# Optimization experiments

Measured on AMD Instinct MI355X. Metric: run time of the kernel, lower is better.

The kernel has to match this reference:

```python
import jax, jax.numpy as jnp
import numpy as np

N = 50000
E = 800000
D_IN, D_HID, D_OUT = 128, 128, 64


def setup_inputs() -> dict:
    key = jax.random.key(0)
    ks = jax.random.split(key, 8)
    x = jax.random.normal(ks[0], (N, D_IN), dtype=jnp.float32)
    edge_index = jax.random.randint(ks[1], (2, E), 0, N, dtype=jnp.int64)
    # Glorot-ish init for weights
    W1 = jax.random.normal(ks[2], (D_IN, D_HID), dtype=jnp.float32) / np.sqrt(D_IN)
    b1 = jnp.zeros((D_HID,), dtype=jnp.float32)
    W2 = jax.random.normal(ks[3], (D_HID, D_OUT), dtype=jnp.float32) / np.sqrt(D_HID)
    b2 = jnp.zeros((D_OUT,), dtype=jnp.float32)
    fc_W = jax.random.normal(ks[4], (D_OUT, D_OUT), dtype=jnp.float32) / np.sqrt(D_OUT)
    fc_b = jnp.zeros((D_OUT,), dtype=jnp.float32)
    return {"x": x, "edge_index": edge_index, "W1": W1, "b1": b1,
            "W2": W2, "b2": b2, "fc_W": fc_W, "fc_b": fc_b}


def _gcn_norm(edge_index, n_nodes):
    # PyG GCNConv default: add self-loops, symmetric normalization
    src, dst = edge_index[0], edge_index[1]
    loops = jnp.arange(n_nodes, dtype=edge_index.dtype)
    src = jnp.concatenate([src, loops])
    dst = jnp.concatenate([dst, loops])
    deg = jax.ops.segment_sum(jnp.ones_like(dst, dtype=jnp.float32), dst,
                              num_segments=n_nodes)
    dinv = jnp.where(deg > 0, jax.lax.rsqrt(deg), 0.0)
    norm = dinv[src] * dinv[dst]  # [E + N]
    return src, dst, norm


def _gcn_conv(x, src, dst, norm, W, b):
    h = x @ W                          # [N, d_out] transform first (fewer FLOPs)
    msg = h[src] * norm[:, None]       # gather + scale  [E+N, d_out]
    out = jax.ops.segment_sum(msg, dst, num_segments=x.shape[0])
    return out + b


def reference(x, edge_index, W1, b1, W2, b2, fc_W, fc_b):
    src, dst, norm = _gcn_norm(edge_index, x.shape[0])
    h = jax.nn.relu(_gcn_conv(x, src, dst, norm, W1, b1))
    h = jax.nn.relu(_gcn_conv(h, src, dst, norm, W2, b2))
    return h @ fc_W + fc_b
```

## Files before the change

kernel.cpp:

```cpp
#include <hip/hip_runtime.h>
#include <hip/hip_bf16.h>


typedef __attribute__((ext_vector_type(8))) short bf16x8;
typedef __attribute__((ext_vector_type(4))) float f32x4;

#define SLAB 64
#define BCAP 6144
#define BINCH 8192

__device__ __forceinline__ unsigned short f2bf(float f) {
    unsigned u = __float_as_uint(f);
    unsigned r = (u + 0x7FFFu + ((u >> 16) & 1u)) >> 16;
    return (unsigned short)r;
}
__device__ __forceinline__ float bf16_lo(unsigned u) {
    return __uint_as_float((u & 0xFFFFu) << 16);
}
__device__ __forceinline__ float bf16_hi(unsigned u) {
    return __uint_as_float(u & 0xFFFF0000u);
}

#define UNPK16(cA, cB, ci)                                        \
    ci[0] = cA.x & 0xFFFFu;  ci[1] = cA.x >> 16;                  \
    ci[2] = cA.y & 0xFFFFu;  ci[3] = cA.y >> 16;                  \
    ci[4] = cA.z & 0xFFFFu;  ci[5] = cA.z >> 16;                  \
    ci[6] = cA.w & 0xFFFFu;  ci[7] = cA.w >> 16;                  \
    ci[8] = cB.x & 0xFFFFu;  ci[9] = cB.x >> 16;                  \
    ci[10] = cB.y & 0xFFFFu; ci[11] = cB.y >> 16;                 \
    ci[12] = cB.z & 0xFFFFu; ci[13] = cB.z >> 16;                 \
    ci[14] = cB.w & 0xFFFFu; ci[15] = cB.w >> 16;


__global__ void k_wt(const float* __restrict__ W1, const float* __restrict__ W2,
                     const float* __restrict__ fcW,
                     unsigned short* __restrict__ W1T, unsigned short* __restrict__ W2T,
                     unsigned short* __restrict__ fcWT, int* __restrict__ gcnt,
                     unsigned short* __restrict__ hs1r, unsigned short* __restrict__ hs2,
                     int n) {
    int j = blockIdx.x * blockDim.x + threadIdx.x;
    if (j < 256) gcnt[j] = 0;
    if (j < 16384) {
        int m = j >> 7, k = j & 127;
        W1T[j] = f2bf(W1[k * 128 + m]);
    } else if (j < 24576) {
        int q = j - 16384;
        int m = q >> 7, k = q & 127;
        W2T[q] = f2bf(W2[k * 64 + m]);
    } else if (j < 28672) {
        int q = j - 24576;
        int m = q >> 6, k = q & 63;
        fcWT[q] = f2bf(fcW[k * 64 + m]);
    } else if (j < 28800) {
        hs1r[(size_t)n * 128 + (j - 28672)] = 0;
    } else if (j < 28864) {
        hs2[(size_t)n * 64 + (j - 28800)] = 0;
    }
}


__device__ __forceinline__ void gemm1_body(const float* __restrict__ X,
                                           const unsigned short* __restrict__ W1T,
                                           unsigned short* __restrict__ outp,
                                           int n, int blk, int tid,
                                           unsigned short* xs) {
    constexpr int LDW = 136;
    int base = blk * 64;
    for (int idx = tid; idx < 64 * 32; idx += 256) {
        int r = idx >> 5, c = idx & 31;
        int row = base + r;
        float4 v = make_float4(0.f, 0.f, 0.f, 0.f);
        if (row < n) v = ((const float4*)X)[(size_t)row * 32 + c];
        unsigned short* dp = &xs[r * LDW + c * 4];
        dp[0] = f2bf(v.x); dp[1] = f2bf(v.y); dp[2] = f2bf(v.z); dp[3] = f2bf(v.w);
    }
    __syncthreads();

    int wave = tid >> 6, lane = tid & 63;
    int quad = lane >> 4, l16 = lane & 15;
    int rbase = wave * 16;

    bf16x8 af[4];
#pragma unroll
    for (int kb = 0; kb < 4; ++kb)
        af[kb] = *(const bf16x8*)&xs[(rbase + l16) * LDW + kb * 32 + quad * 8];

#pragma unroll
    for (int jt = 0; jt < 8; ++jt) {
        f32x4 acc = {0.f, 0.f, 0.f, 0.f};
#pragma unroll
        for (int kb = 0; kb < 4; ++kb) {
            bf16x8 bf = *(const bf16x8*)&W1T[(size_t)(jt * 16 + l16) * 128 + kb * 32 + quad * 8];
            acc = __builtin_amdgcn_mfma_f32_16x16x32_bf16(af[kb], bf, acc, 0, 0, 0);
        }
#pragma unroll
        for (int r = 0; r < 4; ++r) {
            int row = base + rbase + quad * 4 + r;
            if (row < n)
                outp[(size_t)row * 128 + jt * 16 + l16] = f2bf(acc[r]);
        }
    }
}


__global__ __launch_bounds__(1024) void k_front(
    const int* __restrict__ src, const int* __restrict__ dst, int e,
    int* __restrict__ gcnt, unsigned* __restrict__ staging,
    const float* __restrict__ x, const unsigned short* __restrict__ W1T,
    unsigned short* __restrict__ hs1r, int n, int nbk, int ngemm) {
    __shared__ __align__(16) unsigned short xs4[4][64 * 136];
    __shared__ int bcnt[256], bpos[256], gofs[256];
    int bid = (int)blockIdx.x, tid = (int)threadIdx.x;

    if (bid < ngemm) {
        int tile = tid >> 8;
        gemm1_body(x, W1T, hs1r, n, bid * 4 + tile, tid & 255, xs4[tile]);
    } else {
        int b0 = bid - ngemm;
        if (tid < 256) { bcnt[tid] = 0; bpos[tid] = 0; }
        __syncthreads();
        int e0 = b0 * BINCH;
        int d[8], s[8];
#pragma unroll
        for (int r = 0; r < 8; ++r) {
            int i = e0 + r * 1024 + tid;
            if (i < e) { d[r] = dst[i]; s[r] = src[i]; } else d[r] = -1;
        }
#pragma unroll
        for (int r = 0; r < 8; ++r)
            if (d[r] >= 0) atomicAdd(&bcnt[d[r] >> 8], 1);
        __syncthreads();
        if (tid < nbk) {
            int c = bcnt[tid];
            gofs[tid] = c ? atomicAdd(&gcnt[tid], c) : 0;
        }
        __syncthreads();
#pragma unroll
        for (int r = 0; r < 8; ++r) {
            if (d[r] >= 0) {
                int b = d[r] >> 8;
                int p = atomicAdd(&bpos[b], 1);
                int idx = gofs[b] + p;
                if (idx < BCAP)
                    staging[(size_t)b * BCAP + idx] =
                        ((unsigned)d[r] << 16) | (unsigned)s[r];
            }
        }
    }
}


__global__ __launch_bounds__(1024) void k_scatter(
    const unsigned* __restrict__ staging, const int* __restrict__ gcnt,
    int* __restrict__ cnt, unsigned short* __restrict__ col,
    float* __restrict__ dinv, unsigned* __restrict__ hs1u, int n) {
    __shared__ int lcnt[256];
    __shared__ __align__(16) unsigned short ls[256 * SLAB];
    __shared__ float sdi[256];
    int b = (int)blockIdx.x, t = (int)threadIdx.x;
    if (t < 256) lcnt[t] = 0;
    unsigned sent2 = (unsigned)n | ((unsigned)n << 16);
    for (int i = t; i < 256 * SLAB / 2; i += 1024) ((unsigned*)ls)[i] = sent2;
    __syncthreads();
    int eb = gcnt[b]; if (eb > BCAP) eb = BCAP;
    const unsigned* sp = staging + (size_t)b * BCAP;
    for (int i = t; i < eb; i += 1024) {
        unsigned pk = sp[i];
        int dl = (int)(pk >> 16) & 255;
        int pos = atomicAdd(&lcnt[dl], 1);
        if (pos < SLAB) ls[(dl << 6) + pos] = (unsigned short)(pk & 0xFFFFu);
    }
    __syncthreads();
    int base = b << 8;
    const uint4* lsv = (const uint4*)ls;
    uint4* gv = (uint4*)(col + ((size_t)base << 6));
    for (int i = t; i < 256 * SLAB / 8; i += 1024) gv[i] = lsv[i];
    if (t < 256) {
        int c = lcnt[t];
        float dv = rsqrtf((float)c + 1.0f);
        sdi[t] = dv;
        cnt[base + t] = c;
        dinv[base + t] = dv;
    }
    __syncthreads();
    int rows = n - base; if (rows > 256) rows = 256; if (rows < 0) rows = 0;
    unsigned* hp = hs1u + ((size_t)base << 6);
    for (int i = t; i < rows * 64; i += 1024) {
        int r = i >> 6;
        unsigned u = hp[i];
        float sc = sdi[r];
        unsigned lo = f2bf(sc * bf16_lo(u));
        unsigned hi = f2bf(sc * bf16_hi(u));
        hp[i] = lo | (hi << 16);
    }
}


__global__ __launch_bounds__(256) void k_aggg128(
    const int* __restrict__ cnt, const unsigned short* __restrict__ col,
    const unsigned short* __restrict__ hs, const float* __restrict__ dinv,
    const float* __restrict__ bias, const unsigned short* __restrict__ W2T,
    unsigned short* __restrict__ hs2, int n) {
    __shared__ __align__(16) unsigned short ys[16 * 136];
    __shared__ float ldi[16];
    int tid = (int)threadIdx.x;
    int w = tid >> 6, lane = tid & 63;
    int q = lane >> 4, l16 = lane & 15;
    int gbase = (int)blockIdx.x * 16;
    const uint4* hp4 = (const uint4*)hs;

    int node = gbase + w * 4 + q;
    int c = cnt[node]; if (c > SLAB) c = SLAB;
    int dm = c;
    int o = __shfl_xor(dm, 16); if (o > dm) dm = o;
    o = __shfl_xor(dm, 32); if (o > dm) dm = o;

    const unsigned short* cp = &col[(size_t)node * SLAB];
    float di = dinv[node];
    int h0 = node < n ? node : n;
    uint4 su = hp4[(size_t)h0 * 16 + l16];
    float a0 = bf16_lo(su.x), a1 = bf16_hi(su.x);
    float a2 = bf16_lo(su.y), a3 = bf16_hi(su.y);
    float a4 = bf16_lo(su.z), a5 = bf16_hi(su.z);
    float a6 = bf16_lo(su.w), a7 = bf16_hi(su.w);

    for (int i = 0; i < dm; i += 16) {
        uint4 cA = *(const uint4*)&cp[i];
        uint4 cB = *(const uint4*)&cp[i + 8];
        unsigned ci[16];
        UNPK16(cA, cB, ci)
        uint4 u[16];
#pragma unroll
        for (int j = 0; j < 16; ++j) u[j] = hp4[(size_t)ci[j] * 16 + l16];
#pragma unroll
        for (int j = 0; j < 16; ++j) {
            a0 += bf16_lo(u[j].x); a1 += bf16_hi(u[j].x);
            a2 += bf16_lo(u[j].y); a3 += bf16_hi(u[j].y);
            a4 += bf16_lo(u[j].z); a5 += bf16_hi(u[j].z);
            a6 += bf16_lo(u[j].w); a7 += bf16_hi(u[j].w);
        }
    }

    float4 bv0 = *(const float4*)&bias[l16 * 8];
    float4 bv1 = *(const float4*)&bias[l16 * 8 + 4];
    float v0 = fmaxf(di * a0 + bv0.x, 0.0f);
    float v1 = fmaxf(di * a1 + bv0.y, 0.0f);
    float v2 = fmaxf(di * a2 + bv0.z, 0.0f);
    float v3 = fmaxf(di * a3 + bv0.w, 0.0f);
    float v4 = fmaxf(di * a4 + bv1.x, 0.0f);
    float v5 = fmaxf(di * a5 + bv1.y, 0.0f);
    float v6 = fmaxf(di * a6 + bv1.z, 0.0f);
    float v7 = fmaxf(di * a7 + bv1.w, 0.0f);
    uint4 ov;
    ov.x = (unsigned)f2bf(v0) | ((unsigned)f2bf(v1) << 16);
    ov.y = (unsigned)f2bf(v2) | ((unsigned)f2bf(v3) << 16);
    ov.z = (unsigned)f2bf(v4) | ((unsigned)f2bf(v5) << 16);
    ov.w = (unsigned)f2bf(v6) | ((unsigned)f2bf(v7) << 16);
    *(uint4*)((char*)ys + (size_t)(w * 4 + q) * 272 + l16 * 16) = ov;
    if (l16 == 0) ldi[w * 4 + q] = di;
    __syncthreads();

    int quad = lane >> 4, l16b = lane & 15;
    bf16x8 a[4];
#pragma unroll
    for (int kb = 0; kb < 4; ++kb)
        a[kb] = *(const bf16x8*)&ys[l16b * 136 + kb * 32 + quad * 8];
    f32x4 acc = {0.f, 0.f, 0.f, 0.f};
#pragma unroll
    for (int kb = 0; kb < 4; ++kb) {
        bf16x8 bf = *(const bf16x8*)&W2T[(size_t)(w * 16 + l16b) * 128 + kb * 32 + quad * 8];
        acc = __builtin_amdgcn_mfma_f32_16x16x32_bf16(a[kb], bf, acc, 0, 0, 0);
    }
#pragma unroll
    for (int r = 0; r < 4; ++r) {
        int lrow = quad * 4 + r;
        int row = gbase + lrow;
        if (row < n)
            hs2[(size_t)row * 64 + w * 16 + l16b] = f2bf(acc[r] * ldi[lrow]);
    }
}


__global__ __launch_bounds__(256) void k_aggg64(
    const int* __restrict__ cnt, const unsigned short* __restrict__ col,
    const unsigned short* __restrict__ hs, const float* __restrict__ dinv,
    const float* __restrict__ bias, const unsigned short* __restrict__ fcWT,
    const float* __restrict__ fcb, float* __restrict__ out, int n) {
    __shared__ __align__(16) unsigned short yt[16 * 72];
    int tid = (int)threadIdx.x;
    int w = tid >> 6, lane = tid & 63;
    int q = lane >> 4, l16 = lane & 15;
    int gbase = (int)blockIdx.x * 16;
    const uint2* hp2 = (const uint2*)hs;

    int node = gbase + w * 4 + q;
    int c = cnt[node]; if (c > SLAB) c = SLAB;
    int dm = c;
    int o = __shfl_xor(dm, 16); if (o > dm) dm = o;
    o = __shfl_xor(dm, 32); if (o > dm) dm = o;

    const unsigned short* cp = &col[(size_t)node * SLAB];
    float di = dinv[node];
    int h0 = node < n ? node : n;
    uint2 su = hp2[(size_t)h0 * 16 + l16];
    float a0 = bf16_lo(su.x), a1 = bf16_hi(su.x);
    float a2 = bf16_lo(su.y), a3 = bf16_hi(su.y);

    for (int i = 0; i < dm; i += 16) {
        uint4 cA = *(const uint4*)&cp[i];
        uint4 cB = *(const uint4*)&cp[i + 8];
        unsigned ci[16];
        UNPK16(cA, cB, ci)
        uint2 u[16];
#pragma unroll
        for (int j = 0; j < 16; ++j) u[j] = hp2[(size_t)ci[j] * 16 + l16];
#pragma unroll
        for (int j = 0; j < 16; ++j) {
            a0 += bf16_lo(u[j].x); a1 += bf16_hi(u[j].x);
            a2 += bf16_lo(u[j].y); a3 += bf16_hi(u[j].y);
        }
    }

    float4 bv = *(const float4*)&bias[l16 * 4];
    float v0 = fmaxf(di * a0 + bv.x, 0.0f);
    float v1 = fmaxf(di * a1 + bv.y, 0.0f);
    float v2 = fmaxf(di * a2 + bv.z, 0.0f);
    float v3 = fmaxf(di * a3 + bv.w, 0.0f);
    uint2 ov;
    ov.x = (unsigned)f2bf(v0) | ((unsigned)f2bf(v1) << 16);
    ov.y = (unsigned)f2bf(v2) | ((unsigned)f2bf(v3) << 16);
    *(uint2*)((char*)yt + (size_t)(w * 4 + q) * 144 + l16 * 8) = ov;
    __syncthreads();

    int quad = lane >> 4, l16b = lane & 15;
    bf16x8 a[2];
#pragma unroll
    for (int kb = 0; kb < 2; ++kb)
        a[kb] = *(const bf16x8*)&yt[l16b * 72 + kb * 32 + quad * 8];
    f32x4 acc = {0.f, 0.f, 0.f, 0.f};
#pragma unroll
    for (int kb = 0; kb < 2; ++kb) {
        bf16x8 bf = *(const bf16x8*)&fcWT[(size_t)(w * 16 + l16b) * 64 + kb * 32 + quad * 8];
        acc = __builtin_amdgcn_mfma_f32_16x16x32_bf16(a[kb], bf, acc, 0, 0, 0);
    }
    float bv2 = fcb[w * 16 + l16b];
#pragma unroll
    for (int r = 0; r < 4; ++r) {
        int row = gbase + quad * 4 + r;
        if (row < n)
            out[(size_t)row * 64 + w * 16 + l16b] = acc[r] + bv2;
    }
}


extern "C" void kernel_launch(void* const* d_in, const int* in_sizes, int n_in,
                              void* d_out, int out_size, void* d_ws, size_t ws_size,
                              hipStream_t stream) {
    const float* x   = (const float*)d_in[0];
    const int*   ei  = (const int*)d_in[1];
    const float* W1  = (const float*)d_in[2];
    const float* b1  = (const float*)d_in[3];
    const float* W2  = (const float*)d_in[4];
    const float* b2  = (const float*)d_in[5];
    const float* fcW = (const float*)d_in[6];
    const float* fcb = (const float*)d_in[7];
    float* out = (float*)d_out;

    const int N = in_sizes[0] / 128;
    const int E = in_sizes[1] / 2;
    const int* src = ei;
    const int* dst = ei + E;

    const int NB    = (N + 255) >> 8;
    const int Npad  = NB << 8;
    const int nbin  = (E + BINCH - 1) / BINCH;
    const int gg64  = (N + 63) / 64;
    const int ngemm = (gg64 + 3) / 4;
    const int nagg  = (N + 15) / 16;

    auto align16 = [](size_t v) { return (v + 15) & ~(size_t)15; };
    char* p = (char*)d_ws;
    int* gcnt = (int*)p;                       p += align16(sizeof(int) * 256);
    unsigned* staging = (unsigned*)p;          p += align16(sizeof(unsigned) * (size_t)NB * BCAP);
    int* cnt = (int*)p;                        p += align16(sizeof(int) * Npad);
    float* dinv = (float*)p;                   p += align16(sizeof(float) * Npad);
    unsigned short* col = (unsigned short*)p;  p += align16(sizeof(unsigned short) * (size_t)Npad * SLAB);
    unsigned short* W1T = (unsigned short*)p;  p += align16(2 * 128 * 128);
    unsigned short* W2T = (unsigned short*)p;  p += align16(2 * 64 * 128);
    unsigned short* fcWT = (unsigned short*)p; p += align16(2 * 64 * 64);
    unsigned short* hs1r = (unsigned short*)p; p += align16(2 * ((size_t)N + 1) * 128);
    unsigned short* hs2 = (unsigned short*)p;  p += align16(2 * ((size_t)N + 1) * 64);

    k_wt<<<114, 256, 0, stream>>>(W1, W2, fcW, W1T, W2T, fcWT, gcnt,
                                  hs1r, hs2, N);

    k_front<<<ngemm + nbin, 1024, 0, stream>>>(src, dst, E, gcnt, staging,
                                               x, W1T, hs1r, N, NB, ngemm);
    k_scatter<<<NB, 1024, 0, stream>>>(staging, gcnt, cnt, col, dinv,
                                       (unsigned*)hs1r, N);

    k_aggg128<<<nagg, 256, 0, stream>>>(cnt, col, hs1r, dinv, b1, W2T, hs2, N);

    k_aggg64<<<nagg, 256, 0, stream>>>(cnt, col, hs2, dinv, b2, fcWT, fcb, out, N);
}
```

Measured before the change: 172.3 us.

## Replace global-atomic edge binning with per-chunk private segments; prefetch column indices

Edge binning now gives each front block its own per-destination-bucket segment in staging, with a per-chunk count array. This removes the global atomic offset counters, the two-pass local count, and the gcnt zeroing. The scatter kernel walks all chunk segments for its bucket, 64 lanes per segment. The aggregation loops also prefetch the next 16 column indices while gathering the current ones. Risks: per-segment capacity (SCAP) overflow silently drops edges, and the staging buffer is larger with scattered reads.

```diff
diff --git a/kernel.cpp b/kernel.cpp
--- a/kernel.cpp
+++ b/kernel.cpp
@@ -6,8 +6,8 @@
 typedef __attribute__((ext_vector_type(4))) float f32x4;
 
 #define SLAB 64
-#define BCAP 6144
-#define BINCH 8192
+#define SCAP 160
+#define NBIN 60
 
 __device__ __forceinline__ unsigned short f2bf(float f) {
     unsigned u = __float_as_uint(f);
@@ -35,11 +35,10 @@
 __global__ void k_wt(const float* __restrict__ W1, const float* __restrict__ W2,
                      const float* __restrict__ fcW,
                      unsigned short* __restrict__ W1T, unsigned short* __restrict__ W2T,
-                     unsigned short* __restrict__ fcWT, int* __restrict__ gcnt,
+                     unsigned short* __restrict__ fcWT,
                      unsigned short* __restrict__ hs1r, unsigned short* __restrict__ hs2,
                      int n) {
     int j = blockIdx.x * blockDim.x + threadIdx.x;
-    if (j < 256) gcnt[j] = 0;
     if (j < 16384) {
         int m = j >> 7, k = j & 127;
         W1T[j] = f2bf(W1[k * 128 + m]);
@@ -105,70 +104,63 @@
 
 __global__ __launch_bounds__(1024) void k_front(
     const int* __restrict__ src, const int* __restrict__ dst, int e,
-    int* __restrict__ gcnt, unsigned* __restrict__ staging,
+    unsigned* __restrict__ staging, int* __restrict__ bincnt,
     const float* __restrict__ x, const unsigned short* __restrict__ W1T,
-    unsigned short* __restrict__ hs1r, int n, int nbk, int ngemm) {
+    unsigned short* __restrict__ hs1r, int n, int nbk, int ngemm, int binch) {
     __shared__ __align__(16) unsigned short xs4[4][64 * 136];
-    __shared__ int bcnt[256], bpos[256], gofs[256];
+    __shared__ int bpos[256];
     int bid = (int)blockIdx.x, tid = (int)threadIdx.x;
 
     if (bid < ngemm) {
         int tile = tid >> 8;
         gemm1_body(x, W1T, hs1r, n, bid * 4 + tile, tid & 255, xs4[tile]);
     } else {
-        int b0 = bid - ngemm;
-        if (tid < 256) { bcnt[tid] = 0; bpos[tid] = 0; }
+        int c = bid - ngemm;
+        if (tid < 256) bpos[tid] = 0;
         __syncthreads();
-        int e0 = b0 * BINCH;
-        int d[8], s[8];
-#pragma unroll
-        for (int r = 0; r < 8; ++r) {
-            int i = e0 + r * 1024 + tid;
-            if (i < e) { d[r] = dst[i]; s[r] = src[i]; } else d[r] = -1;
-        }
-#pragma unroll
-        for (int r = 0; r < 8; ++r)
-            if (d[r] >= 0) atomicAdd(&bcnt[d[r] >> 8], 1);
+        int e0 = c * binch;
+        int lim = e - e0; if (lim > binch) lim = binch; if (lim < 0) lim = 0;
+        for (int i = tid; i < lim; i += 1024) {
+            int d = dst[e0 + i], s = src[e0 + i];
+            int b = d >> 8;
+            int p = atomicAdd(&bpos[b], 1);
+            if (p < SCAP)
+                staging[((size_t)c * nbk + b) * SCAP + p] =
+                    ((unsigned)d << 16) | (unsigned)s;
+        }
         __syncthreads();
         if (tid < nbk) {
-            int c = bcnt[tid];
-            gofs[tid] = c ? atomicAdd(&gcnt[tid], c) : 0;
-        }
-        __syncthreads();
-#pragma unroll
-        for (int r = 0; r < 8; ++r) {
-            if (d[r] >= 0) {
-                int b = d[r] >> 8;
-                int p = atomicAdd(&bpos[b], 1);
-                int idx = gofs[b] + p;
-                if (idx < BCAP)
-                    staging[(size_t)b * BCAP + idx] =
-                        ((unsigned)d[r] << 16) | (unsigned)s[r];
-            }
+            int v = bpos[tid];
+            bincnt[c * nbk + tid] = v < SCAP ? v : SCAP;
         }
     }
 }
 
 
 __global__ __launch_bounds__(1024) void k_scatter(
-    const unsigned* __restrict__ staging, const int* __restrict__ gcnt,
+    const unsigned* __restrict__ staging, const int* __restrict__ bincnt,
     int* __restrict__ cnt, unsigned short* __restrict__ col,
-    float* __restrict__ dinv, unsigned* __restrict__ hs1u, int n) {
+    float* __restrict__ dinv, unsigned* __restrict__ hs1u, int n, int nbk, int nbin) {
     __shared__ int lcnt[256];
     __shared__ __align__(16) unsigned short ls[256 * SLAB];
     __shared__ float sdi[256];
+    __shared__ int scnt[64];
     int b = (int)blockIdx.x, t = (int)threadIdx.x;
     if (t < 256) lcnt[t] = 0;
+    if (t < nbin) scnt[t] = bincnt[t * nbk + b];
     unsigned sent2 = (unsigned)n | ((unsigned)n << 16);
     for (int i = t; i < 256 * SLAB / 2; i += 1024) ((unsigned*)ls)[i] = sent2;
     __syncthreads();
-    int eb = gcnt[b]; if (eb > BCAP) eb = BCAP;
-    const unsigned* sp = staging + (size_t)b * BCAP;
-    for (int i = t; i < eb; i += 1024) {
-        unsigned pk = sp[i];
-        int dl = (int)(pk >> 16) & 255;
-        int pos = atomicAdd(&lcnt[dl], 1);
-        if (pos < SLAB) ls[(dl << 6) + pos] = (unsigned short)(pk & 0xFFFFu);
+    int g = t >> 6, l = t & 63;
+    for (int c = g; c < nbin; c += 16) {
+        int ccnt = scnt[c];
+        const unsigned* seg = staging + ((size_t)c * nbk + b) * SCAP;
+        for (int i = l; i < ccnt; i += 64) {
+            unsigned pk = seg[i];
+            int dl = (int)(pk >> 16) & 255;
+            int pos = atomicAdd(&lcnt[dl], 1);
+            if (pos < SLAB) ls[(dl << 6) + pos] = (unsigned short)(pk & 0xFFFFu);
+        }
     }
     __syncthreads();
     int base = b << 8;
@@ -224,9 +216,12 @@
     float a4 = bf16_lo(su.z), a5 = bf16_hi(su.z);
     float a6 = bf16_lo(su.w), a7 = bf16_hi(su.w);
 
+    uint4 cA = *(const uint4*)&cp[0];
+    uint4 cB = *(const uint4*)&cp[8];
     for (int i = 0; i < dm; i += 16) {
-        uint4 cA = *(const uint4*)&cp[i];
-        uint4 cB = *(const uint4*)&cp[i + 8];
+        int nx = (i + 16) & 63;
+        uint4 nA = *(const uint4*)&cp[nx];
+        uint4 nB = *(const uint4*)&cp[nx + 8];
         unsigned ci[16];
         UNPK16(cA, cB, ci)
         uint4 u[16];
@@ -239,6 +234,7 @@
             a4 += bf16_lo(u[j].z); a5 += bf16_hi(u[j].z);
             a6 += bf16_lo(u[j].w); a7 += bf16_hi(u[j].w);
         }
+        cA = nA; cB = nB;
     }
 
     float4 bv0 = *(const float4*)&bias[l16 * 8];
@@ -306,9 +302,12 @@
     float a0 = bf16_lo(su.x), a1 = bf16_hi(su.x);
     float a2 = bf16_lo(su.y), a3 = bf16_hi(su.y);
 
+    uint4 cA = *(const uint4*)&cp[0];
+    uint4 cB = *(const uint4*)&cp[8];
     for (int i = 0; i < dm; i += 16) {
-        uint4 cA = *(const uint4*)&cp[i];
-        uint4 cB = *(const uint4*)&cp[i + 8];
+        int nx = (i + 16) & 63;
+        uint4 nA = *(const uint4*)&cp[nx];
+        uint4 nB = *(const uint4*)&cp[nx + 8];
         unsigned ci[16];
         UNPK16(cA, cB, ci)
         uint2 u[16];
@@ -319,6 +318,7 @@
             a0 += bf16_lo(u[j].x); a1 += bf16_hi(u[j].x);
             a2 += bf16_lo(u[j].y); a3 += bf16_hi(u[j].y);
         }
+        cA = nA; cB = nB;
     }
 
     float4 bv = *(const float4*)&bias[l16 * 4];
@@ -373,15 +373,16 @@
 
     const int NB    = (N + 255) >> 8;
     const int Npad  = NB << 8;
-    const int nbin  = (E + BINCH - 1) / BINCH;
+    const int nbin  = NBIN;
+    const int binch = (E + nbin - 1) / nbin;
     const int gg64  = (N + 63) / 64;
     const int ngemm = (gg64 + 3) / 4;
     const int nagg  = (N + 15) / 16;
 
     auto align16 = [](size_t v) { return (v + 15) & ~(size_t)15; };
     char* p = (char*)d_ws;
-    int* gcnt = (int*)p;                       p += align16(sizeof(int) * 256);
-    unsigned* staging = (unsigned*)p;          p += align16(sizeof(unsigned) * (size_t)NB * BCAP);
+    unsigned* staging = (unsigned*)p;          p += align16(sizeof(unsigned) * (size_t)nbin * NB * SCAP);
+    int* bincnt = (int*)p;                     p += align16(sizeof(int) * (size_t)nbin * NB);
     int* cnt = (int*)p;                        p += align16(sizeof(int) * Npad);
     float* dinv = (float*)p;                   p += align16(sizeof(float) * Npad);
     unsigned short* col = (unsigned short*)p;  p += align16(sizeof(unsigned short) * (size_t)Npad * SLAB);
@@ -391,13 +392,13 @@
     unsigned short* hs1r = (unsigned short*)p; p += align16(2 * ((size_t)N + 1) * 128);
     unsigned short* hs2 = (unsigned short*)p;  p += align16(2 * ((size_t)N + 1) * 64);
 
-    k_wt<<<114, 256, 0, stream>>>(W1, W2, fcW, W1T, W2T, fcWT, gcnt,
-                                  hs1r, hs2, N);
-
-    k_front<<<ngemm + nbin, 1024, 0, stream>>>(src, dst, E, gcnt, staging,
-                                               x, W1T, hs1r, N, NB, ngemm);
-    k_scatter<<<NB, 1024, 0, stream>>>(staging, gcnt, cnt, col, dinv,
-                                       (unsigned*)hs1r, N);
+    k_wt<<<114, 256, 0, stream>>>(W1, W2, fcW, W1T, W2T, fcWT, hs1r, hs2, N);
+
+    k_front<<<ngemm + nbin, 1024, 0, stream>>>(src, dst, E, staging, bincnt,
+                                               x, W1T, hs1r, N, NB, ngemm, binch);
+
+    k_scatter<<<NB, 1024, 0, stream>>>(staging, bincnt, cnt, col, dinv,
+                                       (unsigned*)hs1r, N, NB, nbin);
 
     k_aggg128<<<nagg, 256, 0, stream>>>(cnt, col, hs1r, dinv, b1, W2T, hs2, N);
 
```

Measured after the change: 181.5 us. 5.3% more time.
